# Optimization experiments

Hardware: AMD Instinct MI355X
Metric: run time of the kernel (lower is better)

## Reference

```python
import jax, jax.numpy as jnp
import numpy as np

IMG = 416                      # image_shape
DIST = 1075.0                  # isocenter_distance
N_ANG = 320                    # 360 / rotation_resolution(=1.125 deg)
N_DET = IMG                    # detector bins
N_SAMP = IMG                   # integration samples per ray
SCALE = 512.0 / 416.0 * 0.03   # self.scale


def _ray_coords():
    """Pixel-space sample coordinates for every (angle, detector, sample).
    Returns cols, rows of shape [N_ANG, N_DET, N_SAMP] and the step length dt."""
    thetas = (jnp.arange(N_ANG, dtype=jnp.float32) * np.float32(2.0 * np.pi / N_ANG))
    half_diag = (IMG / 2.0) * np.sqrt(2.0)
    gamma_max = np.float32(np.arcsin(half_diag / DIST))  # half fan angle covering image
    gammas = jnp.linspace(-gamma_max, gamma_max, N_DET, dtype=jnp.float32)
    ray_len = np.float32(IMG * np.sqrt(2.0))             # chord length through image
    ts = jnp.linspace(np.float32(DIST - ray_len / 2.0),
                      np.float32(DIST + ray_len / 2.0), N_SAMP, dtype=jnp.float32)
    dt = float(ray_len / (N_SAMP - 1))

    th = thetas[:, None, None]        # [A,1,1]
    gm = gammas[None, :, None]        # [1,D,1]
    t = ts[None, None, :]             # [1,1,S]
    # source position on circle of radius DIST, ray direction toward detector
    sx = np.float32(DIST) * jnp.cos(th)
    sy = np.float32(DIST) * jnp.sin(th)
    x = sx - t * jnp.cos(th + gm)     # [A,D,S] world coords (isocenter at origin)
    y = sy - t * jnp.sin(th + gm)
    ctr = np.float32((IMG - 1) / 2.0)
    return x + ctr, y + ctr, dt       # pixel (col, row) coordinates


def _bilinear(img, cols, rows):
    """Zero-padded bilinear sampling of img[H,W] at float (row,col) coords."""
    c0 = jnp.floor(cols)
    r0 = jnp.floor(rows)
    wc = cols - c0
    wr = rows - r0
    c0i = c0.astype(jnp.int32)
    r0i = r0.astype(jnp.int32)

    def g(ri, ci):
        inb = (ri >= 0) & (ri < IMG) & (ci >= 0) & (ci < IMG)
        v = img[jnp.clip(ri, 0, IMG - 1), jnp.clip(ci, 0, IMG - 1)]
        return jnp.where(inb, v, jnp.float32(0.0))

    return (g(r0i, c0i) * (1 - wr) * (1 - wc)
            + g(r0i, c0i + 1) * (1 - wr) * wc
            + g(r0i + 1, c0i) * wr * (1 - wc)
            + g(r0i + 1, c0i + 1) * wr * wc)


def fan_beam_fp(vol):
    """vol: [B,H,W] -> sinogram [B, N_ANG, N_DET] via ray integration."""
    cols, rows, dt = _ray_coords()
    proj_one = lambda img: _bilinear(img, cols, rows).sum(axis=-1) * jnp.float32(dt)
    return jax.vmap(proj_one)(vol)


def setup_inputs() -> dict:
    key = jax.random.key(0)
    k1, k2 = jax.random.split(key)
    inp = jax.random.normal(k1, (1, 1, IMG, IMG), dtype=jnp.float32)
    tgt = jax.random.normal(k2, (1, 1, IMG, IMG), dtype=jnp.float32)
    return {"input": inp, "target": tgt}


def reference(input, target):
    input_proj = fan_beam_fp(input[:, 0])   # squeeze(1)
    target_proj = fan_beam_fp(target[:, 0])
    return jnp.mean((input_proj - target_proj) ** 2) * jnp.float32(SCALE)
```

## Files before the change

### kernel.cpp

```cpp
#include <hip/hip_runtime.h>
#include <math.h>

#define IMG 416
#define N_ANG 320
#define N_DET 416
#define N_SAMP 416

#define GQSTRIDE 424
#define GQROWS   420
#define GQWORDS  (GQROWS * GQSTRIDE)
#define GQBYTES  ((size_t)GQWORDS * 4)

#define SPLANE  (N_ANG * N_DET)
#define SBYTES  ((size_t)SPLANE * 4)
#define WSNEED  (GQBYTES + SBYTES)

#define LSTRIDE 116
#define LWORDS  (108 * LSTRIDE)

typedef float vfloat2 __attribute__((ext_vector_type(2)));

__global__ __launch_bounds__(256) void pack_kernel(const float* __restrict__ a,
                                                   const float* __restrict__ b,
                                                   unsigned int* __restrict__ Gq,
                                                   float* __restrict__ S,
                                                   float* __restrict__ out) {
    int i = blockIdx.x * 256 + threadIdx.x;
    if (i == 0) out[0] = 0.0f;
    if (i < SPLANE) S[i] = 0.0f;
    if (i >= GQWORDS) return;
    int row  = i / GQSTRIDE;
    int colw = i - row * GQSTRIDE;
    int pr = row - 2, pc = colw - 2;
    auto D = [&](int r, int c) -> float {
        if ((unsigned)r < (unsigned)IMG && (unsigned)c < (unsigned)IMG) {
            int idx = r * IMG + c;
            return a[idx] - b[idx];
        }
        return 0.0f;
    };
    const float v00 = D(pr, pc),     v01 = D(pr, pc + 1);
    const float v10 = D(pr + 1, pc), v11 = D(pr + 1, pc + 1);
    unsigned int u = __builtin_amdgcn_cvt_pk_fp8_f32(v00, v01, 0u, false);
    u = __builtin_amdgcn_cvt_pk_fp8_f32(v10, v11, u, true);
    Gq[i] = u;
}

__global__ void zero_out_kernel(float* __restrict__ out) {
    if (threadIdx.x == 0) out[0] = 0.0f;
}

__global__ __launch_bounds__(448) void proj_lds(const unsigned int* __restrict__ Gq,
                                                float* __restrict__ S,
                                                float theta_step, float gmax,
                                                float gstep, float t0,
                                                float dtstep) {
    __shared__ unsigned int Lw[LWORDS];

    const int blk  = blockIdx.x;
    const int a    = blk >> 4;
    const int tile = blk & 15;
    const int qi = tile >> 2, qj = tile & 3;
    const int r0 = 104 * qi - 2;
    const int c0 = 104 * qj - 2;

    {
        const uint4* __restrict__ src =
            (const uint4*)(Gq + (r0 + 2) * GQSTRIDE + (c0 + 2));
        for (int i = threadIdx.x; i < 108 * 27; i += 448) {
            int rr = i / 27, cc = i - rr * 27;
            uint4 w = src[rr * (GQSTRIDE / 4) + cc];
            *(uint4*)&Lw[rr * LSTRIDE + cc * 4] = w;
        }
    }
    __syncthreads();

    const int d = threadIdx.x;
    if (d < N_DET) {
        const float theta = (float)a * theta_step;
        const float gamma = fmaf((float)d, gstep, -gmax);
        float s1, c1, s2, c2;
        sincosf(theta, &s1, &c1);
        sincosf(theta + gamma, &s2, &c2);
        const float sx = fmaf(1075.0f, c1, 207.5f);
        const float sy = fmaf(1075.0f, s1, 207.5f);

        const float C0 = fmaf(-t0, c2, sx), dc = dtstep * c2;
        const float R0 = fmaf(-t0, s2, sy), dr = dtstep * s2;

        const float cl = (qj == 0) ? -1.0f : 104.0f * qj;
        const float ch = (qj == 3) ? 416.0f : 104.0f * (qj + 1);
        const float rl = (qi == 0) ? -1.0f : 104.0f * qi;
        const float rh = (qi == 3) ? 416.0f : 104.0f * (qi + 1);

        int klo = 0, khi = N_SAMP - 1;
        auto clip1 = [&](float X0, float dX, float lo, float hi) {
            if (fabsf(dX) < 1e-8f) {
                if (!(X0 >= lo && X0 < hi)) { klo = 1; khi = 0; }
            } else {
                const float inv = 1.0f / dX;
                float x1 = (X0 - hi) * inv;
                float x2 = (X0 - lo) * inv;
                x1 = fminf(fmaxf(x1, -1e6f), 1e6f);
                x2 = fminf(fmaxf(x2, -1e6f), 1e6f);
                int lo_k, hi_k;
                if (dX > 0.0f) { lo_k = (int)floorf(x1) + 1; hi_k = (int)floorf(x2); }
                else           { lo_k = (int)ceilf(x2);      hi_k = (int)ceilf(x1) - 1; }
                klo = max(klo, lo_k);
                khi = min(khi, hi_k);
            }
        };
        clip1(C0, dc, cl, ch);
        clip1(R0, dr, rl, rh);

        if (klo <= khi) {
            float colR = fmaf(-(float)klo, dc, C0) - (float)c0;
            float rowR = fmaf(-(float)klo, dr, R0) - (float)r0;
            float acc = 0.0f;
            #pragma unroll 4
            for (int k = klo; k <= khi; ++k) {
                const int ci = (int)colR;
                const int ri = (int)rowR;
                const float wc = colR - (float)ci;
                const float wr = rowR - (float)ri;
                const unsigned int u = Lw[ri * LSTRIDE + ci];
                const vfloat2 lo2 = __builtin_amdgcn_cvt_pk_f32_fp8(u, false);
                const vfloat2 hi2 = __builtin_amdgcn_cvt_pk_f32_fp8(u, true);
                const float top = fmaf(wc, lo2[1] - lo2[0], lo2[0]);
                const float bot = fmaf(wc, hi2[1] - hi2[0], hi2[0]);
                acc = fmaf(wr, bot - top, acc + top);
                colR -= dc;
                rowR -= dr;
            }
            atomicAdd(&S[a * N_DET + d], acc);
        }
    }
}

__global__ __launch_bounds__(256) void reduce_kernel(const float* __restrict__ S,
                                                     float* __restrict__ out,
                                                     float coef) {
    const int i = blockIdx.x * 256 + threadIdx.x;
    float v = (i < SPLANE) ? S[i] : 0.0f;
    float sq = v * v;
    #pragma unroll
    for (int m = 32; m > 0; m >>= 1) sq += __shfl_down(sq, m, 64);
    __shared__ float w[4];
    const int lane = threadIdx.x & 63;
    if (lane == 0) w[threadIdx.x >> 6] = sq;
    __syncthreads();
    if (threadIdx.x == 0)
        atomicAdd(out, (w[0] + w[1] + w[2] + w[3]) * coef);
}

__global__ __launch_bounds__(256) void proj_fused(const float* __restrict__ imgA,
                                                  const float* __restrict__ imgB,
                                                  float* __restrict__ out,
                                                  float theta_step, float gmax,
                                                  float gstep, float t0,
                                                  float dtstep, float coef) {
    const int idx = blockIdx.x * 256 + threadIdx.x;
    const int a  = idx / N_DET;
    const int dd = idx - a * N_DET;
    const float theta = (float)a * theta_step;
    const float gamma = fmaf((float)dd, gstep, -gmax);
    float s1, c1, s2, c2;
    sincosf(theta, &s1, &c1);
    sincosf(theta + gamma, &s2, &c2);
    const float sx = 1075.0f * c1 + 207.5f;
    const float sy = 1075.0f * s1 + 207.5f;
    float acc = 0.0f;
    #pragma unroll 4
    for (int s = 0; s < N_SAMP; ++s) {
        const float t   = fmaf((float)s, dtstep, t0);
        const float col = fmaf(-t, c2, sx);
        const float row = fmaf(-t, s2, sy);
        const float c0 = floorf(col);
        const float r0 = floorf(row);
        const float wc = col - c0;
        const float wr = row - r0;
        const int ci = (int)c0;
        const int ri = (int)r0;
        auto Gv = [&](int r, int c) -> float {
            if ((unsigned)r < (unsigned)IMG && (unsigned)c < (unsigned)IMG)
                return imgA[r * IMG + c] - imgB[r * IMG + c];
            return 0.0f;
        };
        const float v00 = Gv(ri, ci);
        const float v01 = Gv(ri, ci + 1);
        const float v10 = Gv(ri + 1, ci);
        const float v11 = Gv(ri + 1, ci + 1);
        const float top = fmaf(wc, v01 - v00, v00);
        const float bot = fmaf(wc, v11 - v10, v10);
        acc += fmaf(wr, bot - top, top);
    }
    float sq = acc * acc;
    #pragma unroll
    for (int o = 32; o > 0; o >>= 1) sq += __shfl_down(sq, o, 64);
    __shared__ float wsum[4];
    const int lane = threadIdx.x & 63;
    if (lane == 0) wsum[threadIdx.x >> 6] = sq;
    __syncthreads();
    if (threadIdx.x == 0)
        atomicAdd(out, (wsum[0] + wsum[1] + wsum[2] + wsum[3]) * coef);
}

extern "C" void kernel_launch(void* const* d_in, const int* in_sizes, int n_in,
                              void* d_out, int out_size, void* d_ws, size_t ws_size,
                              hipStream_t stream) {
    const float* in = (const float*)d_in[0];
    const float* tg = (const float*)d_in[1];
    float* out = (float*)d_out;

    const double half_diag = (IMG / 2.0) * sqrt(2.0);
    const double ray_len   = IMG * sqrt(2.0);
    const float  gmax      = (float)asin(half_diag / 1075.0);
    const float  gstep     = (float)(2.0 * (double)gmax / (N_DET - 1));
    const float  t0        = (float)(1075.0 - ray_len / 2.0);
    const float  dtstep    = (float)(ray_len / (N_SAMP - 1));
    const float  theta_step = (float)(2.0 * M_PI / N_ANG);
    const double dt        = ray_len / (N_SAMP - 1);
    const double SCALE     = 512.0 / 416.0 * 0.03;
    const float  coef      = (float)(dt * dt * SCALE / ((double)N_ANG * N_DET));

    if (ws_size >= WSNEED) {
        unsigned int* Gq = (unsigned int*)d_ws;
        float* S = (float*)((char*)d_ws + GQBYTES);
        pack_kernel<<<(GQWORDS + 255) / 256, 256, 0, stream>>>(in, tg, Gq, S, out);
        proj_lds<<<N_ANG * 16, 448, 0, stream>>>(Gq, S, theta_step, gmax, gstep,
                                                 t0, dtstep);
        reduce_kernel<<<(SPLANE + 255) / 256, 256, 0, stream>>>(S, out, coef);
    } else {
        zero_out_kernel<<<1, 64, 0, stream>>>(out);
        proj_fused<<<(N_ANG * N_DET) / 256, 256, 0, stream>>>(
            in, tg, out, theta_step, gmax, gstep, t0, dtstep, coef);
    }
}
```

Baseline: 124.7 us.

## Switch to horizontal fp8 pair packing with 16-bit LDS fetches and larger tiles

The packed difference image now stores horizontally overlapping fp8 pixel pairs (two pairs per 32-bit word), so each sample reads two 16-bit LDS values (top and bottom row) instead of one 2x2 quad word. This halves the packed image footprint, which lets each block cover a 208x104 tile and halves the block count, and so the number of partial-sum atomics. The cost is two LDS loads per sample instead of one, scalar 32-bit staging loads instead of uint4, and a larger LDS tile per block that may limit occupancy.

```diff
diff --git a/kernel.cpp b/kernel.cpp
--- a/kernel.cpp
+++ b/kernel.cpp
@@ -6,71 +6,72 @@
 #define N_DET 416
 #define N_SAMP 416
 
-#define GQSTRIDE 424
-#define GQROWS   420
-#define GQWORDS  (GQROWS * GQSTRIDE)
-#define GQBYTES  ((size_t)GQWORDS * 4)
+#define GPROWS   432
+#define GPSTRIDE_W 216
+#define GPWORDS  (GPROWS * GPSTRIDE_W)
+#define GPBYTES  ((size_t)GPWORDS * 4)
 
 #define SPLANE  (N_ANG * N_DET)
-#define SBYTES  ((size_t)SPLANE * 4)
-#define WSNEED  (GQBYTES + SBYTES)
-
-#define LSTRIDE 116
-#define LWORDS  (108 * LSTRIDE)
+#define S1BYTES ((size_t)SPLANE * 4)
+#define WSNEED  (GPBYTES + S1BYTES)
+
+#define LSTRIDE_W  55
+#define LSTRIDE_PX 110
+#define LROWS      216
+#define LWORDS     (LROWS * LSTRIDE_W)
+
+#define NBLK (N_ANG * 8)
 
 typedef float vfloat2 __attribute__((ext_vector_type(2)));
 
 __global__ __launch_bounds__(256) void pack_kernel(const float* __restrict__ a,
                                                    const float* __restrict__ b,
-                                                   unsigned int* __restrict__ Gq,
+                                                   unsigned int* __restrict__ Gp,
                                                    float* __restrict__ S,
                                                    float* __restrict__ out) {
     int i = blockIdx.x * 256 + threadIdx.x;
     if (i == 0) out[0] = 0.0f;
     if (i < SPLANE) S[i] = 0.0f;
-    if (i >= GQWORDS) return;
-    int row  = i / GQSTRIDE;
-    int colw = i - row * GQSTRIDE;
-    int pr = row - 2, pc = colw - 2;
-    auto D = [&](int r, int c) -> float {
-        if ((unsigned)r < (unsigned)IMG && (unsigned)c < (unsigned)IMG) {
-            int idx = r * IMG + c;
-            return a[idx] - b[idx];
-        }
+    if (i >= GPWORDS) return;
+    int row = i / GPSTRIDE_W;
+    int wc  = i - row * GPSTRIDE_W;
+    int r  = row - 8;
+    int c0 = wc * 2 - 8;
+    auto D = [&](int rr, int cc) -> float {
+        if ((unsigned)rr < (unsigned)IMG && (unsigned)cc < (unsigned)IMG)
+            return a[rr * IMG + cc] - b[rr * IMG + cc];
         return 0.0f;
     };
-    const float v00 = D(pr, pc),     v01 = D(pr, pc + 1);
-    const float v10 = D(pr + 1, pc), v11 = D(pr + 1, pc + 1);
-    unsigned int u = __builtin_amdgcn_cvt_pk_fp8_f32(v00, v01, 0u, false);
-    u = __builtin_amdgcn_cvt_pk_fp8_f32(v10, v11, u, true);
-    Gq[i] = u;
+    const float v0 = D(r, c0), v1 = D(r, c0 + 1), v2 = D(r, c0 + 2);
+    unsigned int u = __builtin_amdgcn_cvt_pk_fp8_f32(v0, v1, 0u, false);
+    u = __builtin_amdgcn_cvt_pk_fp8_f32(v1, v2, u, true);
+    Gp[i] = u;
 }
 
 __global__ void zero_out_kernel(float* __restrict__ out) {
     if (threadIdx.x == 0) out[0] = 0.0f;
 }
 
-__global__ __launch_bounds__(448) void proj_lds(const unsigned int* __restrict__ Gq,
+__global__ __launch_bounds__(448) void proj_lds(const unsigned int* __restrict__ Gp,
                                                 float* __restrict__ S,
                                                 float theta_step, float gmax,
                                                 float gstep, float t0,
                                                 float dtstep) {
     __shared__ unsigned int Lw[LWORDS];
 
-    const int blk  = blockIdx.x;
-    const int a    = blk >> 4;
-    const int tile = blk & 15;
+    const int blk = blockIdx.x;
+    const int a    = blk >> 3;
+    const int tile = blk & 7;
     const int qi = tile >> 2, qj = tile & 3;
-    const int r0 = 104 * qi - 2;
-    const int c0 = 104 * qj - 2;
+    const int r0s = 208 * qi - 4;
+    const int c0s = 104 * qj - 4;
 
     {
-        const uint4* __restrict__ src =
-            (const uint4*)(Gq + (r0 + 2) * GQSTRIDE + (c0 + 2));
-        for (int i = threadIdx.x; i < 108 * 27; i += 448) {
-            int rr = i / 27, cc = i - rr * 27;
-            uint4 w = src[rr * (GQSTRIDE / 4) + cc];
-            *(uint4*)&Lw[rr * LSTRIDE + cc * 4] = w;
+        const int gbase = (r0s + 8) * GPSTRIDE_W + (52 * qj + 2);
+        for (int i = threadIdx.x; i < LWORDS; i += 448) {
+            int rr = i / LSTRIDE_W;
+            int cc = i - rr * LSTRIDE_W;
+            Lw[rr * LSTRIDE_W + cc] = Gp[gbase + rr * GPSTRIDE_W + cc];
         }
     }
     __syncthreads();
@@ -90,8 +91,8 @@
 
         const float cl = (qj == 0) ? -1.0f : 104.0f * qj;
         const float ch = (qj == 3) ? 416.0f : 104.0f * (qj + 1);
-        const float rl = (qi == 0) ? -1.0f : 104.0f * qi;
-        const float rh = (qi == 3) ? 416.0f : 104.0f * (qi + 1);
+        const float rl = (qi == 0) ? -1.0f : 208.0f;
+        const float rh = (qi == 0) ? 208.0f : 416.0f;
 
         int klo = 0, khi = N_SAMP - 1;
         auto clip1 = [&](float X0, float dX, float lo, float hi) {
@@ -114,8 +115,9 @@
         clip1(R0, dr, rl, rh);
 
         if (klo <= khi) {
-            float colR = fmaf(-(float)klo, dc, C0) - (float)c0;
-            float rowR = fmaf(-(float)klo, dr, R0) - (float)r0;
+            float colR = fmaf(-(float)klo, dc, C0) - (float)c0s;
+            float rowR = fmaf(-(float)klo, dr, R0) - (float)r0s;
+            const unsigned short* __restrict__ Lp = (const unsigned short*)Lw;
             float acc = 0.0f;
             #pragma unroll 4
             for (int k = klo; k <= khi; ++k) {
@@ -123,11 +125,13 @@
                 const int ri = (int)rowR;
                 const float wc = colR - (float)ci;
                 const float wr = rowR - (float)ri;
-                const unsigned int u = Lw[ri * LSTRIDE + ci];
-                const vfloat2 lo2 = __builtin_amdgcn_cvt_pk_f32_fp8(u, false);
-                const vfloat2 hi2 = __builtin_amdgcn_cvt_pk_f32_fp8(u, true);
-                const float top = fmaf(wc, lo2[1] - lo2[0], lo2[0]);
-                const float bot = fmaf(wc, hi2[1] - hi2[0], hi2[0]);
+                const int base = ri * LSTRIDE_PX + ci;
+                const unsigned int ptop = Lp[base];
+                const unsigned int pbot = Lp[base + LSTRIDE_PX];
+                const vfloat2 t2 = __builtin_amdgcn_cvt_pk_f32_fp8(ptop, false);
+                const vfloat2 b2 = __builtin_amdgcn_cvt_pk_f32_fp8(pbot, false);
+                const float top = fmaf(wc, t2[1] - t2[0], t2[0]);
+                const float bot = fmaf(wc, b2[1] - b2[0], b2[0]);
                 acc = fmaf(wr, bot - top, acc + top);
                 colR -= dc;
                 rowR -= dr;
@@ -224,11 +228,11 @@
     const float  coef      = (float)(dt * dt * SCALE / ((double)N_ANG * N_DET));
 
     if (ws_size >= WSNEED) {
-        unsigned int* Gq = (unsigned int*)d_ws;
-        float* S = (float*)((char*)d_ws + GQBYTES);
-        pack_kernel<<<(GQWORDS + 255) / 256, 256, 0, stream>>>(in, tg, Gq, S, out);
-        proj_lds<<<N_ANG * 16, 448, 0, stream>>>(Gq, S, theta_step, gmax, gstep,
-                                                 t0, dtstep);
+        unsigned int* Gp = (unsigned int*)d_ws;
+        float* S = (float*)((char*)d_ws + GPBYTES);
+        pack_kernel<<<(SPLANE + 255) / 256, 256, 0, stream>>>(in, tg, Gp, S, out);
+        proj_lds<<<NBLK, 448, 0, stream>>>(Gp, S, theta_step, gmax, gstep,
+                                           t0, dtstep);
         reduce_kernel<<<(SPLANE + 255) / 256, 256, 0, stream>>>(S, out, coef);
     } else {
         zero_out_kernel<<<1, 64, 0, stream>>>(out);
```

Result: faster. 112.9 us (-9.5%).
